# Kernel optimization log

Measured on AMD Instinct MI355X. Metric: run time of the kernel, lower is better.

The kernel has to match this reference:

```python
import jax, jax.numpy as jnp
from jax import lax
import numpy as np

V, Dm, L, B = 32000, 1024, 1024, 4      # vocab, d_model, seq_len, batch
NL, E, H = 2, 8, 1024                    # layers, experts, expert_hidden
DS, DC, EXP = 16, 4, 2                   # d_state, d_conv, expand
DI = EXP * Dm                            # d_inner = 2048
DTR = Dm // 16                           # dt_rank = 64


def setup_inputs() -> dict:
    key = jax.random.key(0)
    ks = iter(jax.random.split(key, 48))
    def n(shape, s=0.02):
        return jax.random.normal(next(ks), shape, jnp.float32) * s
    inp = {
        "tokens": jax.random.randint(next(ks), (B, L), 1, V),
        "emb": jax.random.uniform(next(ks), (V, Dm), jnp.float32, -0.1, 0.1),
        "pos": n((1, L, Dm)),
        # per-layer stacked Mamba params
        "in_w": n((NL, 2 * DI, Dm)),
        "conv_w": n((NL, DI, 1, DC), 0.1),
        "conv_b": jnp.zeros((NL, DI)),
        "xp_w": n((NL, DTR + 2 * DS, DI)),
        "dt_w": n((NL, DI, DTR), 0.1),
        "dt_b": jnp.zeros((NL, DI)),
        "A_log": jnp.log(jnp.tile(jnp.arange(1, DS + 1, dtype=jnp.float32)[None, None, :], (NL, DI, 1))),
        "D_ssm": jnp.ones((NL, DI)),
        "out_w": n((NL, Dm, DI)),
        # layer norms
        "ln1_g": jnp.ones((NL, Dm)), "ln1_b": jnp.zeros((NL, Dm)),
        "ln2_g": jnp.ones((NL, Dm)), "ln2_b": jnp.zeros((NL, Dm)),
        # MoE
        "gate_w": n((NL, E, Dm)), "gate_b": jnp.zeros((NL, E)),
        "e_w1": n((NL, E, H, Dm)), "e_b1": jnp.zeros((NL, E, H)),
        "e_w2": n((NL, E, Dm, H)), "e_b2": jnp.zeros((NL, E, Dm)),
        # head
        "fc1_w": jax.random.uniform(next(ks), (128, Dm), jnp.float32, -0.1, 0.1),
        "fc1_b": jnp.zeros((128,)),
        "fc2_w": jax.random.uniform(next(ks), (2, 128), jnp.float32, -0.1, 0.1),
        "fc2_b": jnp.zeros((2,)),
    }
    return inp


def _ln(x, g, b, eps=1e-5):
    m = x.mean(-1, keepdims=True)
    v = ((x - m) ** 2).mean(-1, keepdims=True)
    return (x - m) * lax.rsqrt(v + eps) * g + b


def _mamba(x, in_w, conv_w, conv_b, xp_w, dt_w, dt_b, A_log, D_ssm, out_w):
    Bb = x.shape[0]
    u, z = jnp.split(x @ in_w.T, 2, axis=-1)  # [B,L,DI] each
    # causal depthwise conv over time
    uc = lax.conv_general_dilated(jnp.swapaxes(u, 1, 2), conv_w, (1,), [(DC - 1, 0)],
                                  feature_group_count=DI,
                                  dimension_numbers=("NCH", "OIH", "NCH")) + conv_b[None, :, None]
    u = jax.nn.silu(jnp.swapaxes(uc, 1, 2))  # [B,L,DI]
    dt, Bm, Cm = jnp.split(u @ xp_w.T, [DTR, DTR + DS], axis=-1)
    dt = jax.nn.softplus(dt @ dt_w.T + dt_b)  # [B,L,DI]
    A = -jnp.exp(A_log)  # [DI,DS]

    def step(h, inp):
        u_t, dt_t, B_t, C_t = inp  # [B,DI],[B,DI],[B,DS],[B,DS]
        h = jnp.exp(dt_t[..., None] * A) * h + (dt_t * u_t)[..., None] * B_t[:, None, :]
        return h, jnp.einsum("bdn,bn->bd", h, C_t)

    h0 = jnp.zeros((Bb, DI, DS), x.dtype)
    xs = tuple(jnp.swapaxes(a, 0, 1) for a in (u, dt, Bm, Cm))
    _, ys = lax.scan(step, h0, xs)
    y = jnp.swapaxes(ys, 0, 1) + u * D_ssm
    return (y * jax.nn.silu(z)) @ out_w.T


def _moe(x, gate_w, gate_b, w1, b1, w2, b2):
    Bb, Ll, Dd = x.shape
    xf = x.reshape(-1, Dd)
    gw = jax.nn.softmax(xf @ gate_w.T + gate_b, axis=-1)  # [N,E]
    top_w = jnp.max(gw, axis=-1)
    top_idx = jnp.argmax(gw, axis=-1)
    out = jnp.zeros_like(xf)
    for e in range(E):  # top-1 routing: only routed tokens keep expert e's output
        ye = jax.nn.relu(xf @ w1[e].T + b1[e]) @ w2[e].T + b2[e]
        out = out + jnp.where((top_idx == e)[:, None], top_w[:, None] * ye, 0.0)
    return out.reshape(Bb, Ll, Dd)


def reference(tokens, emb, pos, in_w, conv_w, conv_b, xp_w, dt_w, dt_b, A_log, D_ssm, out_w,
              ln1_g, ln1_b, ln2_g, ln2_b, gate_w, gate_b, e_w1, e_b1, e_w2, e_b2,
              fc1_w, fc1_b, fc2_w, fc2_b):
    x = emb[tokens] + pos[:, :tokens.shape[1], :]
    for l in range(NL):
        x = x + _ln(_mamba(x, in_w[l], conv_w[l], conv_b[l], xp_w[l], dt_w[l], dt_b[l],
                           A_log[l], D_ssm[l], out_w[l]), ln1_g[l], ln1_b[l])
        x = x + _ln(_moe(x, gate_w[l], gate_b[l], e_w1[l], e_b1[l], e_w2[l], e_b2[l]),
                    ln2_g[l], ln2_b[l])
    mask = (x.sum(-1) != 0)[..., None].astype(x.dtype)
    pooled = (x * mask).sum(1) / jnp.maximum(mask.sum(1), 1.0)
    h = jax.nn.relu(pooled @ fc1_w.T + fc1_b)
    return h @ fc2_w.T + fc2_b
```

## Files before the change

### kernel.cpp

```cpp
#include <hip/hip_runtime.h>
#include <hip/hip_bf16.h>

using bf = __hip_bfloat16;
typedef unsigned short u16;

#define V_   32000
#define DM   1024
#define LQ   1024
#define BB   4
#define NLAY 2
#define NE   8
#define HH   1024
#define DS   16
#define DC   4
#define DI   2048
#define DTR  64
#define NTOK (BB*LQ)

#define NC 8
#define CL (LQ/NC)

typedef __attribute__((ext_vector_type(8))) short s8v;
typedef __attribute__((ext_vector_type(4))) float f4v;

__device__ inline float tofl(float x) { return x; }
__device__ inline float tofl(bf x) { return __bfloat162float(x); }

template<typename T> __device__ inline T fromf(float v);
template<> __device__ inline float fromf<float>(float v) { return v; }
template<> __device__ inline bf fromf<bf>(float v) { return __float2bfloat16(v); }

__device__ inline u16 f2bfu(float x) {
    bf h = __float2bfloat16(x);
    return __builtin_bit_cast(u16, h);
}
__device__ inline float bfu2f(u16 u) {
    bf h = __builtin_bit_cast(bf, u);
    return __bfloat162float(h);
}

__device__ inline f4v mfma16(s8v a, s8v b, f4v c) {
    return __builtin_amdgcn_mfma_f32_16x16x32_bf16(a, b, c, 0, 0, 0);
}

__device__ __forceinline__ void gl2lds16(const u16* g, u16* l) {
    __builtin_amdgcn_global_load_lds(
        (const __attribute__((address_space(1))) unsigned int*)g,
        (__attribute__((address_space(3))) unsigned int*)l, 16, 0, 0);
}

__global__ __launch_bounds__(256) void split2_kernel(
    const float* __restrict__ in, int ldin,
    u16* __restrict__ out, int K)
{
    int id = blockIdx.x * 256 + threadIdx.x;
    int e4 = id * 4;
    int r = e4 / K;
    int k = e4 - r * K;
    float4 v = *(const float4*)(in + (size_t)r * ldin + k);
    int b = k >> 5, j = k & 31;
    ushort4 hi, lo;
    hi.x = f2bfu(v.x); lo.x = f2bfu(v.x - bfu2f(hi.x));
    hi.y = f2bfu(v.y); lo.y = f2bfu(v.y - bfu2f(hi.y));
    hi.z = f2bfu(v.z); lo.z = f2bfu(v.z - bfu2f(hi.z));
    hi.w = f2bfu(v.w); lo.w = f2bfu(v.w - bfu2f(hi.w));
    u16* o = out + (size_t)r * (2 * K) + b * 64 + j;
    *(ushort4*)o = hi;
    *(ushort4*)(o + 32) = lo;
}

__global__ __launch_bounds__(256) void zerof4_kernel(float4* __restrict__ p) {
    p[(size_t)blockIdx.x * 256 + threadIdx.x] = make_float4(0.f, 0.f, 0.f, 0.f);
}

template<typename TC, int TERMS, int BN>
__global__ __launch_bounds__(256, 3) void gemm_s(
    const u16* __restrict__ A, int lda,
    const u16* __restrict__ Bw, int ldb,
    TC* __restrict__ C, int ldc,
    int M, int N, int K32,
    const float* __restrict__ bias, int epi,
    const int* __restrict__ cnt, const int* __restrict__ offs,
    const int* __restrict__ perm, int permmode,
    const float* __restrict__ scale,
    long long strideB_e, long long stride_bias_e,
    int nqz, int atomic_out)
{
    int zb = blockIdx.z;
    int Meff = M, rowoff = 0;
    int q0 = 0, q1 = K32;
    if (cnt) {
        Meff = cnt[zb];
        rowoff = offs[zb];
        Bw += (size_t)zb * strideB_e;
        if (bias) bias += (size_t)zb * stride_bias_e;
    } else if (nqz) {
        q0 = zb * nqz; q1 = q0 + nqz;
    }
    int m0 = blockIdx.y * 128;
    if (m0 >= Meff) return;
    int n0 = blockIdx.x * BN;

    constexpr int MI  = (BN == 128) ? 4 : 2;
    constexpr int NBR = BN / 64;

    __shared__ u16 AsH[128 * 32];
    __shared__ u16 AsL[(TERMS == 3) ? 128 * 32 : 8];
    __shared__ u16 BsH[BN * 32];
    __shared__ u16 BsL[BN * 32];

    int t = threadIdx.x, lane = t & 63, wv = t >> 6;
    int wm = (BN == 128) ? (wv & 1) * 64 : wv * 32;
    int wn = (BN == 128) ? (wv >> 1) * 64 : 0;
    int fr = lane & 15, kq = lane >> 4;
    int chunk = lane & 3;

    int arow[2], brow[2];
#pragma unroll
    for (int r = 0; r < 2; r++) {
        int m = m0 + r * 64 + wv * 16 + (lane >> 2);
        int ar = rowoff + ((m < Meff) ? m : 0);
        arow[r] = (permmode & 1) ? perm[ar] : ar;
    }
#pragma unroll
    for (int r = 0; r < NBR; r++) {
        int n = n0 + r * 64 + wv * 16 + (lane >> 2);
        brow[r] = (n < N) ? n : 0;
    }

    f4v acc[MI][4];
#pragma unroll
    for (int i = 0; i < MI; i++)
#pragma unroll
        for (int j = 0; j < 4; j++) acc[i][j] = 0.f;

    for (int q = q0; q < q1; ++q) {
        size_t acol = (TERMS == 3) ? ((size_t)q * 64 + chunk * 8)
                                   : ((size_t)q * 32 + chunk * 8);
        size_t bcol = (size_t)q * 64 + chunk * 8;
#pragma unroll
        for (int r = 0; r < 2; r++) {
            const u16* ap = A + (size_t)arow[r] * lda + acol;
            gl2lds16(ap, &AsH[(r * 64 + wv * 16) * 32]);
            if constexpr (TERMS == 3)
                gl2lds16(ap + 32, &AsL[(r * 64 + wv * 16) * 32]);
        }
#pragma unroll
        for (int r = 0; r < NBR; r++) {
            const u16* bp = Bw + (size_t)brow[r] * ldb + bcol;
            gl2lds16(bp, &BsH[(r * 64 + wv * 16) * 32]);
            gl2lds16(bp + 32, &BsL[(r * 64 + wv * 16) * 32]);
        }
        __syncthreads();

        s8v ahf[MI], bhf[4], blf[4];
#pragma unroll
        for (int mi = 0; mi < MI; mi++)
            ahf[mi] = *(const s8v*)&AsH[(wm + mi * 16 + fr) * 32 + kq * 8];
#pragma unroll
        for (int ni = 0; ni < 4; ni++)
            bhf[ni] = *(const s8v*)&BsH[(wn + ni * 16 + fr) * 32 + kq * 8];
#pragma unroll
        for (int ni = 0; ni < 4; ni++)
            blf[ni] = *(const s8v*)&BsL[(wn + ni * 16 + fr) * 32 + kq * 8];
#pragma unroll
        for (int mi = 0; mi < MI; mi++)
#pragma unroll
            for (int ni = 0; ni < 4; ni++) {
                acc[mi][ni] = mfma16(ahf[mi], bhf[ni], acc[mi][ni]);
                acc[mi][ni] = mfma16(ahf[mi], blf[ni], acc[mi][ni]);
            }
        if constexpr (TERMS == 3) {
            s8v alf[MI];
#pragma unroll
            for (int mi = 0; mi < MI; mi++)
                alf[mi] = *(const s8v*)&AsL[(wm + mi * 16 + fr) * 32 + kq * 8];
#pragma unroll
            for (int mi = 0; mi < MI; mi++)
#pragma unroll
                for (int ni = 0; ni < 4; ni++)
                    acc[mi][ni] = mfma16(alf[mi], bhf[ni], acc[mi][ni]);
        }
        __syncthreads();
    }

#pragma unroll
    for (int mi = 0; mi < MI; mi++) {
#pragma unroll
        for (int r4 = 0; r4 < 4; r4++) {
            int m = m0 + wm + mi * 16 + kq * 4 + r4;
            if (m >= Meff) continue;
            long long crow;
            float sc = 1.f;
            int ar = rowoff + m;
            if (permmode & 2) { int tok = perm[ar]; crow = tok; sc = scale[tok]; }
            else crow = ar;
#pragma unroll
            for (int ni = 0; ni < 4; ni++) {
                int n = n0 + wn + ni * 16 + fr;
                if (n >= N) continue;
                float v = acc[mi][ni][r4];
                if (bias) v += bias[n];
                if (epi == 1) v = (v > 20.f) ? v : log1pf(__expf(v));
                else if (epi == 2) v = fmaxf(v, 0.f);
                v *= sc;
                long long idx = crow * ldc + n;
                if constexpr (sizeof(TC) == 4) {
                    if (atomic_out) atomicAdd((float*)C + idx, v);
                    else C[idx] = fromf<TC>(v);
                } else {
                    C[idx] = fromf<TC>(v);
                }
            }
        }
    }
}

__global__ __launch_bounds__(256) void embed_kernel(
    const int* __restrict__ tokens, const float* __restrict__ emb,
    const float* __restrict__ pos, float* __restrict__ X)
{
    int id = blockIdx.x * 256 + threadIdx.x;
    int r = id >> 10, d = id & 1023;
    int l = r & (LQ - 1);
    int tok = tokens[r];
    X[id] = emb[(size_t)tok * DM + d] + pos[l * DM + d];
}

__global__ __launch_bounds__(256) void conv_kernel(
    const bf* __restrict__ XZ, const float* __restrict__ cw,
    const float* __restrict__ cb, bf* __restrict__ UC)
{
    int id = blockIdx.x * 256 + threadIdx.x;
    int d = id & (DI - 1);
    int r = id >> 11;
    int l = r & (LQ - 1);
    float acc = cb[d];
#pragma unroll
    for (int j = 0; j < DC; j++) {
        int ll = l - (DC - 1) + j;
        if (ll >= 0)
            acc += tofl(XZ[(size_t)(r - (DC - 1) + j) * (2 * DI) + d]) * cw[d * DC + j];
    }
    float sg = 1.f / (1.f + __expf(-acc));
    UC[id] = __float2bfloat16(acc * sg);
}

template<int PHASE>
__global__ __launch_bounds__(256) void scan_chunk(
    const bf* __restrict__ UC, float* __restrict__ DT,
    const float* __restrict__ W96, const bf* __restrict__ XZ,
    const float* __restrict__ A_log, const float* __restrict__ D_ssm,
    float* __restrict__ Hout, float* __restrict__ Stot,
    const float* __restrict__ Hin)
{
    int d = blockIdx.x * 256 + threadIdx.x;
    int c = blockIdx.y, b = blockIdx.z;
    float A[DS];
#pragma unroll
    for (int n = 0; n < DS; n++) A[n] = -__expf(A_log[d * DS + n]);
    float Dv = D_ssm[d];
    float h[DS];
    size_t hbase = ((size_t)(b * DI + d) * NC + c) * DS;
    if (PHASE == 0) {
#pragma unroll
        for (int n = 0; n < DS; n++) h[n] = 0.f;
    } else {
#pragma unroll
        for (int n = 0; n < DS; n += 4)
            *(float4*)&h[n] = *(const float4*)&Hin[hbase + n];
    }
    float S = 0.f;

    for (int t = 0; t < CL; t++) {
        int r = (b << 10) + c * CL + t;
        float u = tofl(UC[(size_t)r * DI + d]);
        float dt = DT[(size_t)r * DI + d];
        float du = dt * u;
        if (PHASE == 0) S += dt;
        float y = 0.f;
#pragma unroll
        for (int n = 0; n < DS; n++) {
            float Bv = W96[r * 96 + DTR + n];
            h[n] = __expf(dt * A[n]) * h[n] + du * Bv;
            if (PHASE == 1) y += h[n] * W96[r * 96 + DTR + DS + n];
        }
        if (PHASE == 1) {
            float z = tofl(XZ[(size_t)r * (2 * DI) + DI + d]);
            float sil = z / (1.f + __expf(-z));
            DT[(size_t)r * DI + d] = (y + u * Dv) * sil;
        }
    }
    if (PHASE == 0) {
#pragma unroll
        for (int n = 0; n < DS; n += 4)
            *(float4*)&Hout[hbase + n] = *(const float4*)&h[n];
        Stot[(size_t)(b * DI + d) * NC + c] = S;
    }
}

__global__ __launch_bounds__(256) void scan_combine(
    const float* __restrict__ Hout, const float* __restrict__ Stot,
    const float* __restrict__ A_log, float* __restrict__ Hin)
{
    int id = blockIdx.x * 256 + threadIdx.x;
    int n = id & (DS - 1);
    int d = (id >> 4) & (DI - 1);
    int b = id >> 15;
    float A = -__expf(A_log[d * DS + n]);
    float h = 0.f;
    size_t base = (size_t)(b * DI + d) * NC * DS + n;
    size_t sbase = (size_t)(b * DI + d) * NC;
    for (int c = 0; c < NC; c++) {
        Hin[base + (size_t)c * DS] = h;
        h = __expf(A * Stot[sbase + c]) * h + Hout[base + (size_t)c * DS];
    }
}

__global__ __launch_bounds__(256) void ln_residual_kernel(
    float* __restrict__ X, const float* __restrict__ src,
    const float* __restrict__ g, const float* __restrict__ b)
{
    int row = blockIdx.x, tid = threadIdx.x;
    __shared__ float red[256];
    float v[4];
    float s = 0.f;
#pragma unroll
    for (int i = 0; i < 4; i++) { v[i] = src[(size_t)row * DM + tid + 256 * i]; s += v[i]; }
    red[tid] = s; __syncthreads();
    for (int o = 128; o > 0; o >>= 1) { if (tid < o) red[tid] += red[tid + o]; __syncthreads(); }
    float mean = red[0] * (1.f / DM);
    __syncthreads();
    float vs = 0.f;
#pragma unroll
    for (int i = 0; i < 4; i++) { float dd = v[i] - mean; vs += dd * dd; }
    red[tid] = vs; __syncthreads();
    for (int o = 128; o > 0; o >>= 1) { if (tid < o) red[tid] += red[tid + o]; __syncthreads(); }
    float rstd = rsqrtf(red[0] * (1.f / DM) + 1e-5f);
#pragma unroll
    for (int i = 0; i < 4; i++) {
        int c = tid + 256 * i;
        X[(size_t)row * DM + c] += (v[i] - mean) * rstd * g[c] + b[c];
    }
}

__global__ __launch_bounds__(64) void gate_kernel(
    const float* __restrict__ X, const float* __restrict__ gw, const float* __restrict__ gb,
    int* __restrict__ top_idx, float* __restrict__ top_w, int* __restrict__ cnt)
{
    int n = blockIdx.x;
    int lane = threadIdx.x;
    float acc[NE] = {};
    for (int k = lane; k < DM; k += 64) {
        float xv = X[(size_t)n * DM + k];
#pragma unroll
        for (int e = 0; e < NE; e++) acc[e] += xv * gw[e * DM + k];
    }
#pragma unroll
    for (int e = 0; e < NE; e++)
        for (int o = 32; o > 0; o >>= 1) acc[e] += __shfl_down(acc[e], o);
    if (lane == 0) {
        float logits[NE];
        float best = -1e30f; int bi = 0;
#pragma unroll
        for (int e = 0; e < NE; e++) {
            logits[e] = acc[e] + gb[e];
            if (logits[e] > best) { best = logits[e]; bi = e; }
        }
        float s = 0.f;
#pragma unroll
        for (int e = 0; e < NE; e++) s += __expf(logits[e] - best);
        top_idx[n] = bi;
        top_w[n] = 1.f / s;
        atomicAdd(&cnt[bi], 1);
    }
}

__global__ void zero8_kernel(int* p) { if (threadIdx.x < 8) p[threadIdx.x] = 0; }

__global__ void offsets_kernel(const int* __restrict__ cnt, int* __restrict__ offs, int* __restrict__ pos)
{
    if (threadIdx.x == 0) {
        int a = 0;
        for (int e = 0; e < NE; e++) { offs[e] = a; a += cnt[e]; pos[e] = 0; }
        offs[NE] = a;
    }
}

__global__ __launch_bounds__(256) void scatter_kernel(
    const int* __restrict__ top_idx, const int* __restrict__ offs,
    int* __restrict__ pos, int* __restrict__ perm)
{
    int n = blockIdx.x * 256 + threadIdx.x;
    if (n >= NTOK) return;
    int e = top_idx[n];
    int slot = atomicAdd(&pos[e], 1);
    perm[offs[e] + slot] = n;
}

__global__ __launch_bounds__(256) void rowmask_kernel(const float* __restrict__ X, float* __restrict__ maskf)
{
    int row = blockIdx.x, tid = threadIdx.x;
    __shared__ float red[256];
    float s = 0.f;
    for (int i = tid; i < DM; i += 256) s += X[(size_t)row * DM + i];
    red[tid] = s; __syncthreads();
    for (int o = 128; o > 0; o >>= 1) { if (tid < o) red[tid] += red[tid + o]; __syncthreads(); }
    if (tid == 0) maskf[row] = (red[0] != 0.f) ? 1.f : 0.f;
}

__global__ __launch_bounds__(256) void cntb_kernel(const float* __restrict__ maskf, float* __restrict__ cntb)
{
    int b = blockIdx.x, tid = threadIdx.x;
    __shared__ float red[256];
    float s = 0.f;
    for (int i = tid; i < LQ; i += 256) s += maskf[b * LQ + i];
    red[tid] = s; __syncthreads();
    for (int o = 128; o > 0; o >>= 1) { if (tid < o) red[tid] += red[tid + o]; __syncthreads(); }
    if (tid == 0) cntb[b] = red[0];
}

__global__ __launch_bounds__(256) void pooled_kernel(
    const float* __restrict__ X, const float* __restrict__ maskf,
    const float* __restrict__ cntb, float* __restrict__ pooled)
{
    int d = blockIdx.x * 256 + threadIdx.x;
    int b = blockIdx.y;
    float s = 0.f;
    for (int l = 0; l < LQ; l++)
        s += X[(size_t)((b << 10) + l) * DM + d] * maskf[(b << 10) + l];
    pooled[b * DM + d] = s / fmaxf(cntb[b], 1.f);
}

__global__ __launch_bounds__(128) void head_kernel(
    const float* __restrict__ pooled,
    const float* __restrict__ fc1w, const float* __restrict__ fc1b,
    const float* __restrict__ fc2w, const float* __restrict__ fc2b,
    float* __restrict__ out)
{
    int b = blockIdx.x;
    int j = threadIdx.x;
    __shared__ float hbuf[128];
    float acc = fc1b[j];
    for (int k = 0; k < DM; k++) acc += pooled[b * DM + k] * fc1w[j * DM + k];
    hbuf[j] = fmaxf(acc, 0.f);
    __syncthreads();
    if (j < 2) {
        float o = fc2b[j];
        for (int k = 0; k < 128; k++) o += hbuf[k] * fc2w[j * 128 + k];
        out[b * 2 + j] = o;
    }
}

extern "C" void kernel_launch(void* const* d_in, const int* in_sizes, int n_in,
                              void* d_out, int out_size, void* d_ws, size_t ws_size,
                              hipStream_t stream)
{
    const int*   tokens = (const int*)d_in[0];
    const float* emb    = (const float*)d_in[1];
    const float* pos    = (const float*)d_in[2];
    const float* in_w   = (const float*)d_in[3];
    const float* conv_w = (const float*)d_in[4];
    const float* conv_b = (const float*)d_in[5];
    const float* xp_w   = (const float*)d_in[6];
    const float* dt_w   = (const float*)d_in[7];
    const float* dt_b   = (const float*)d_in[8];
    const float* A_log  = (const float*)d_in[9];
    const float* D_ssm  = (const float*)d_in[10];
    const float* out_w  = (const float*)d_in[11];
    const float* ln1_g  = (const float*)d_in[12];
    const float* ln1_b  = (const float*)d_in[13];
    const float* ln2_g  = (const float*)d_in[14];
    const float* ln2_b  = (const float*)d_in[15];
    const float* gate_w = (const float*)d_in[16];
    const float* gate_b = (const float*)d_in[17];
    const float* e_w1   = (const float*)d_in[18];
    const float* e_b1   = (const float*)d_in[19];
    const float* e_w2   = (const float*)d_in[20];
    const float* e_b2   = (const float*)d_in[21];
    const float* fc1_w  = (const float*)d_in[22];
    const float* fc1_b  = (const float*)d_in[23];
    const float* fc2_w  = (const float*)d_in[24];
    const float* fc2_b  = (const float*)d_in[25];
    float* outp = (float*)d_out;

    char* wsb = (char*)d_ws;
    size_t off = 0;
    auto alloc = [&](size_t bytes) { char* p = wsb + off; off += (bytes + 255) & ~(size_t)255; return p; };
    float* X    = (float*)alloc((size_t)NTOK * DM * 4);
    char* xzraw = (char*)alloc((size_t)NTOK * 2 * DI * 2);
    char* ucraw = (char*)alloc((size_t)NTOK * DI * 2);
    float* W96  = (float*)alloc((size_t)NTOK * 96 * 4);
    char* dtraw = (char*)alloc((size_t)NTOK * DI * 4);
    float* Hout = (float*)alloc((size_t)BB * DI * NC * DS * 4);
    float* Hin  = (float*)alloc((size_t)BB * DI * NC * DS * 4);
    float* Stot = (float*)alloc((size_t)BB * DI * NC * 4);
    float* top_w  = (float*)alloc(NTOK * 4);
    float* maskf  = (float*)alloc(NTOK * 4);
    float* pooled = (float*)alloc(BB * DM * 4);
    float* cntb   = (float*)alloc(64);
    int* top_idx  = (int*)alloc(NTOK * 4);
    int* perm     = (int*)alloc(NTOK * 4);
    int* cnt      = (int*)alloc(64);
    int* offs     = (int*)alloc(64);
    int* posc     = (int*)alloc(64);

    bf*    XZ   = (bf*)xzraw;
    bf*    UC   = (bf*)ucraw;
    float* DT   = (float*)dtraw;
    u16*   XS   = (u16*)ucraw;
    u16*   DTS  = (u16*)xzraw;
    float* H1   = (float*)xzraw;
    u16*   H1S  = (u16*)(xzraw + (size_t)NTOK * HH * 4);
    float* MAM1 = (float*)ucraw;
    float* MAM2 = (float*)xzraw;
    u16*   WB   = (u16*)dtraw;
    u16*   WDT  = (u16*)Hin;
    u16*   W96S = (u16*)Hout;

    embed_kernel<<<(NTOK * DM) / 256, 256, 0, stream>>>(tokens, emb, pos, X);

    for (int lay = 0; lay < NLAY; lay++) {
        const float* in_w_l   = in_w   + (size_t)lay * 2 * DI * DM;
        const float* conv_w_l = conv_w + (size_t)lay * DI * DC;
        const float* conv_b_l = conv_b + (size_t)lay * DI;
        const float* xp_w_l   = xp_w   + (size_t)lay * 96 * DI;
        const float* dt_w_l   = dt_w   + (size_t)lay * DI * DTR;
        const float* dt_b_l   = dt_b   + (size_t)lay * DI;
        const float* A_log_l  = A_log  + (size_t)lay * DI * DS;
        const float* D_ssm_l  = D_ssm  + (size_t)lay * DI;
        const float* out_w_l  = out_w  + (size_t)lay * DM * DI;
        const float* gate_w_l = gate_w + (size_t)lay * NE * DM;
        const float* gate_b_l = gate_b + (size_t)lay * NE;
        const float* e_w1_l   = e_w1   + (size_t)lay * NE * HH * DM;
        const float* e_b1_l   = e_b1   + (size_t)lay * NE * HH;
        const float* e_w2_l   = e_w2   + (size_t)lay * NE * DM * HH;
        const float* e_b2_l   = e_b2   + (size_t)lay * NE * DM;

        split2_kernel<<<(NTOK * DM) / 1024, 256, 0, stream>>>(X, DM, XS, DM);
        split2_kernel<<<(2 * DI * DM) / 1024, 256, 0, stream>>>(in_w_l, DM, WB, DM);
        gemm_s<bf, 3, 128><<<dim3(32, 32, 1), 256, 0, stream>>>(
            XS, 2 * DM, WB, 2 * DM, XZ, 2 * DI, NTOK, 2 * DI, DM / 32,
            nullptr, 0, nullptr, nullptr, nullptr, 0, nullptr, 0, 0, 0, 0);

        conv_kernel<<<(NTOK * DI) / 256, 256, 0, stream>>>(XZ, conv_w_l, conv_b_l, UC);

        zerof4_kernel<<<(NTOK * 96) / 1024, 256, 0, stream>>>((float4*)W96);
        split2_kernel<<<(96 * DI) / 1024, 256, 0, stream>>>(xp_w_l, DI, WB, DI);
        gemm_s<float, 2, 128><<<dim3(1, 32, 8), 256, 0, stream>>>(
            (const u16*)UC, DI, WB, 2 * DI, W96, 96, NTOK, 96, DI / 32,
            nullptr, 0, nullptr, nullptr, nullptr, 0, nullptr, 0, 0, (DI / 32) / 8, 1);

        split2_kernel<<<(DI * DTR) / 1024, 256, 0, stream>>>(dt_w_l, DTR, WDT, DTR);
        split2_kernel<<<(NTOK * DTR) / 1024, 256, 0, stream>>>(W96, 96, W96S, DTR);
        gemm_s<float, 3, 128><<<dim3(16, 32, 1), 256, 0, stream>>>(
            W96S, 2 * DTR, WDT, 2 * DTR, DT, DI, NTOK, DI, DTR / 32,
            dt_b_l, 1, nullptr, nullptr, nullptr, 0, nullptr, 0, 0, 0, 0);

        scan_chunk<0><<<dim3(DI / 256, NC, BB), 256, 0, stream>>>(
            UC, DT, W96, XZ, A_log_l, D_ssm_l, Hout, Stot, nullptr);
        scan_combine<<<(BB * DI * DS) / 256, 256, 0, stream>>>(Hout, Stot, A_log_l, Hin);
        scan_chunk<1><<<dim3(DI / 256, NC, BB), 256, 0, stream>>>(
            UC, DT, W96, XZ, A_log_l, D_ssm_l, Hout, Stot, Hin);

        split2_kernel<<<(NTOK * DI) / 1024, 256, 0, stream>>>(DT, DI, DTS, DI);
        split2_kernel<<<(DM * DI) / 1024, 256, 0, stream>>>(out_w_l, DI, WB, DI);
        gemm_s<float, 3, 64><<<dim3(16, 32, 1), 256, 0, stream>>>(
            DTS, 2 * DI, WB, 2 * DI, MAM1, DM, NTOK, DM, DI / 32,
            nullptr, 0, nullptr, nullptr, nullptr, 0, nullptr, 0, 0, 0, 0);

        ln_residual_kernel<<<NTOK, 256, 0, stream>>>(X, MAM1, ln1_g + lay * DM, ln1_b + lay * DM);

        zero8_kernel<<<1, 32, 0, stream>>>(cnt);
        gate_kernel<<<NTOK, 64, 0, stream>>>(X, gate_w_l, gate_b_l, top_idx, top_w, cnt);
        offsets_kernel<<<1, 1, 0, stream>>>(cnt, offs, posc);
        scatter_kernel<<<NTOK / 256, 256, 0, stream>>>(top_idx, offs, posc, perm);

        split2_kernel<<<(NTOK * DM) / 1024, 256, 0, stream>>>(X, DM, XS, DM);
        split2_kernel<<<((size_t)NE * HH * DM) / 1024, 256, 0, stream>>>(e_w1_l, DM, WB, DM);
        gemm_s<float, 3, 64><<<dim3(16, 32, NE), 256, 0, stream>>>(
            XS, 2 * DM, WB, 2 * DM, H1, HH, NTOK, HH, DM / 32,
            e_b1_l, 2, cnt, offs, perm, 1, nullptr,
            (long long)HH * 2 * DM, (long long)HH, 0, 0);

        split2_kernel<<<(NTOK * HH) / 1024, 256, 0, stream>>>(H1, HH, H1S, HH);
        split2_kernel<<<((size_t)NE * DM * HH) / 1024, 256, 0, stream>>>(e_w2_l, HH, WB, HH);
        gemm_s<float, 3, 64><<<dim3(16, 32, NE), 256, 0, stream>>>(
            H1S, 2 * HH, WB, 2 * HH, MAM2, DM, NTOK, DM, HH / 32,
            e_b2_l, 0, cnt, offs, perm, 2, top_w,
            (long long)DM * 2 * HH, (long long)DM, 0, 0);

        ln_residual_kernel<<<NTOK, 256, 0, stream>>>(X, MAM2, ln2_g + lay * DM, ln2_b + lay * DM);
    }

    rowmask_kernel<<<NTOK, 256, 0, stream>>>(X, maskf);
    cntb_kernel<<<BB, 256, 0, stream>>>(maskf, cntb);
    pooled_kernel<<<dim3(DM / 256, BB, 1), 256, 0, stream>>>(X, maskf, cntb, pooled);
    head_kernel<<<BB, 128, 0, stream>>>(pooled, fc1_w, fc1_b, fc2_w, fc2_b, outp);
}
```

Baseline: 1.881 ms.

## Add pipelined in-proj GEMM, fuse bf16 splits into epilogues, widen scan chunks

Adds a 512-thread, 256x128-tile GEMM for the input projection. It uses triple-buffered direct global-to-LDS loads, swizzled LDS reads and raised priority around the MFMA block. The hi/lo bf16 split of the activations moves into the layernorm-residual epilogue and the expert-1 GEMM epilogue, which removes separate split passes and the H1 fp32 buffer. Counter zeroing is folded into layernorm, the scan uses 16 chunks with next-step loads prefetched, and the out-proj and expert GEMMs use BN=128 tiles. The new GEMM drops bounds checks, so it assumes tile-divisible shapes.

```diff
diff --git a/kernel.cpp b/kernel.cpp
--- a/kernel.cpp
+++ b/kernel.cpp
@@ -17,7 +17,7 @@
 #define DTR  64
 #define NTOK (BB*LQ)
 
-#define NC 8
+#define NC 16
 #define CL (LQ/NC)
 
 typedef __attribute__((ext_vector_type(8))) short s8v;
@@ -73,7 +73,98 @@
     p[(size_t)blockIdx.x * 256 + threadIdx.x] = make_float4(0.f, 0.f, 0.f, 0.f);
 }
 
-template<typename TC, int TERMS, int BN>
+__global__ __launch_bounds__(512) void gemm_pipe3(
+    const u16* __restrict__ A, int lda,
+    const u16* __restrict__ Bw, int ldb,
+    bf* __restrict__ C, int ldc,
+    int K32)
+{
+    __shared__ u16 LA[3][256 * 64];
+    __shared__ u16 LB[3][128 * 64];
+
+    int t = threadIdx.x, lane = t & 63, wv = t >> 6;
+    int m0 = blockIdx.y * 256, n0 = blockIdx.x * 128;
+    int wm = (wv >> 1) * 64, wn = (wv & 1) * 64;
+    int fr = lane & 15, kq = lane >> 4;
+
+    int lrow8 = lane >> 3;
+    int lchunk = (lane & 7) ^ lrow8;
+    const u16* Abase = A + (size_t)(m0 + wv * 32 + lrow8) * lda + lchunk * 8;
+    const u16* Bbase = Bw + (size_t)(n0 + wv * 16 + lrow8) * ldb + lchunk * 8;
+
+    f4v acc[4][4];
+#pragma unroll
+    for (int i = 0; i < 4; i++)
+#pragma unroll
+        for (int j = 0; j < 4; j++) acc[i][j] = 0.f;
+
+    auto stage = [&](int q, int s) {
+        const u16* ap = Abase + (size_t)q * 64;
+#pragma unroll
+        for (int j = 0; j < 4; j++)
+            gl2lds16(ap + (size_t)(j * 8) * lda, &LA[s][(wv * 32 + j * 8) * 64]);
+        const u16* bp = Bbase + (size_t)q * 64;
+#pragma unroll
+        for (int j = 0; j < 2; j++)
+            gl2lds16(bp + (size_t)(j * 8) * ldb, &LB[s][(wv * 16 + j * 8) * 64]);
+    };
+
+    stage(0, 0);
+    stage(1, 1);
+
+    for (int q = 0; q < K32; ++q) {
+        int s = q % 3;
+        if (q + 1 < K32) asm volatile("s_waitcnt vmcnt(6)" ::: "memory");
+        else             asm volatile("s_waitcnt vmcnt(0)" ::: "memory");
+        __builtin_amdgcn_sched_barrier(0);
+        __builtin_amdgcn_s_barrier();
+        __builtin_amdgcn_sched_barrier(0);
+
+        if (q + 2 < K32) stage(q + 2, (q + 2) % 3);
+
+        s8v ah[4], al[4], bh[4], bl[4];
+#pragma unroll
+        for (int mi = 0; mi < 4; mi++) {
+            int R = wm + mi * 16 + fr;
+            int c = kq ^ (R & 7);
+            ah[mi] = *(const s8v*)&LA[s][R * 64 + c * 8];
+            al[mi] = *(const s8v*)&LA[s][R * 64 + (c ^ 4) * 8];
+        }
+#pragma unroll
+        for (int ni = 0; ni < 4; ni++) {
+            int R = wn + ni * 16 + fr;
+            int c = kq ^ (R & 7);
+            bh[ni] = *(const s8v*)&LB[s][R * 64 + c * 8];
+            bl[ni] = *(const s8v*)&LB[s][R * 64 + (c ^ 4) * 8];
+        }
+        __builtin_amdgcn_s_setprio(1);
+#pragma unroll
+        for (int mi = 0; mi < 4; mi++)
+#pragma unroll
+            for (int ni = 0; ni < 4; ni++) {
+                acc[mi][ni] = mfma16(ah[mi], bh[ni], acc[mi][ni]);
+                acc[mi][ni] = mfma16(ah[mi], bl[ni], acc[mi][ni]);
+                acc[mi][ni] = mfma16(al[mi], bh[ni], acc[mi][ni]);
+            }
+        __builtin_amdgcn_s_setprio(0);
+        __builtin_amdgcn_sched_barrier(0);
+    }
+
+#pragma unroll
+    for (int mi = 0; mi < 4; mi++) {
+#pragma unroll
+        for (int r4 = 0; r4 < 4; r4++) {
+            int m = m0 + wm + mi * 16 + kq * 4 + r4;
+#pragma unroll
+            for (int ni = 0; ni < 4; ni++) {
+                int n = n0 + wn + ni * 16 + fr;
+                C[(size_t)m * ldc + n] = __float2bfloat16(acc[mi][ni][r4]);
+            }
+        }
+    }
+}
+
+template<typename TC, int TERMS, int BN, int SPLITOUT = 0>
 __global__ __launch_bounds__(256, 3) void gemm_s(
     const u16* __restrict__ A, int lda,
     const u16* __restrict__ Bw, int ldb,
@@ -204,12 +295,20 @@
                 if (epi == 1) v = (v > 20.f) ? v : log1pf(__expf(v));
                 else if (epi == 2) v = fmaxf(v, 0.f);
                 v *= sc;
-                long long idx = crow * ldc + n;
-                if constexpr (sizeof(TC) == 4) {
-                    if (atomic_out) atomicAdd((float*)C + idx, v);
-                    else C[idx] = fromf<TC>(v);
+                if constexpr (SPLITOUT) {
+                    u16 hi = f2bfu(v);
+                    u16 lo = f2bfu(v - bfu2f(hi));
+                    size_t o = (size_t)crow * ldc + ((n >> 5) << 6) + (n & 31);
+                    ((u16*)C)[o] = hi;
+                    ((u16*)C)[o + 32] = lo;
                 } else {
-                    C[idx] = fromf<TC>(v);
+                    long long idx = crow * ldc + n;
+                    if constexpr (sizeof(TC) == 4) {
+                        if (atomic_out) atomicAdd((float*)C + idx, v);
+                        else C[idx] = fromf<TC>(v);
+                    } else {
+                        C[idx] = fromf<TC>(v);
+                    }
                 }
             }
         }
@@ -272,24 +371,32 @@
     }
     float S = 0.f;
 
+    size_t rowb = (size_t)((b << 10) + c * CL);
+    float u_c = tofl(UC[rowb * DI + d]);
+    float dt_c = DT[rowb * DI + d];
+
     for (int t = 0; t < CL; t++) {
-        int r = (b << 10) + c * CL + t;
-        float u = tofl(UC[(size_t)r * DI + d]);
-        float dt = DT[(size_t)r * DI + d];
-        float du = dt * u;
-        if (PHASE == 0) S += dt;
+        size_t r = rowb + t;
+        float u_n = 0.f, dt_n = 0.f;
+        if (t + 1 < CL) {
+            u_n = tofl(UC[(r + 1) * DI + d]);
+            dt_n = DT[(r + 1) * DI + d];
+        }
+        float du = dt_c * u_c;
+        if (PHASE == 0) S += dt_c;
         float y = 0.f;
 #pragma unroll
         for (int n = 0; n < DS; n++) {
             float Bv = W96[r * 96 + DTR + n];
-            h[n] = __expf(dt * A[n]) * h[n] + du * Bv;
+            h[n] = __expf(dt_c * A[n]) * h[n] + du * Bv;
             if (PHASE == 1) y += h[n] * W96[r * 96 + DTR + DS + n];
         }
         if (PHASE == 1) {
-            float z = tofl(XZ[(size_t)r * (2 * DI) + DI + d]);
+            float z = tofl(XZ[r * (2 * DI) + DI + d]);
             float sil = z / (1.f + __expf(-z));
-            DT[(size_t)r * DI + d] = (y + u * Dv) * sil;
-        }
+            DT[r * DI + d] = (y + u_c * Dv) * sil;
+        }
+        u_c = u_n; dt_c = dt_n;
     }
     if (PHASE == 0) {
 #pragma unroll
@@ -319,7 +426,8 @@
 
 __global__ __launch_bounds__(256) void ln_residual_kernel(
     float* __restrict__ X, const float* __restrict__ src,
-    const float* __restrict__ g, const float* __restrict__ b)
+    const float* __restrict__ g, const float* __restrict__ b,
+    u16* __restrict__ xs, int* __restrict__ cntz)
 {
     int row = blockIdx.x, tid = threadIdx.x;
     __shared__ float red[256];
@@ -340,8 +448,17 @@
 #pragma unroll
     for (int i = 0; i < 4; i++) {
         int c = tid + 256 * i;
-        X[(size_t)row * DM + c] += (v[i] - mean) * rstd * g[c] + b[c];
-    }
+        float nx = X[(size_t)row * DM + c] + (v[i] - mean) * rstd * g[c] + b[c];
+        X[(size_t)row * DM + c] = nx;
+        if (xs) {
+            u16 hi = f2bfu(nx);
+            u16 lo = f2bfu(nx - bfu2f(hi));
+            size_t o2 = (size_t)row * (2 * DM) + ((c >> 5) << 6) + (c & 31);
+            xs[o2] = hi;
+            xs[o2 + 32] = lo;
+        }
+    }
+    if (cntz && row == 0 && tid < 8) cntz[tid] = 0;
 }
 
 __global__ __launch_bounds__(64) void gate_kernel(
@@ -375,8 +492,6 @@
         atomicAdd(&cnt[bi], 1);
     }
 }
-
-__global__ void zero8_kernel(int* p) { if (threadIdx.x < 8) p[threadIdx.x] = 0; }
 
 __global__ void offsets_kernel(const int* __restrict__ cnt, int* __restrict__ offs, int* __restrict__ pos)
 {
@@ -510,7 +625,6 @@
     float* DT   = (float*)dtraw;
     u16*   XS   = (u16*)ucraw;
     u16*   DTS  = (u16*)xzraw;
-    float* H1   = (float*)xzraw;
     u16*   H1S  = (u16*)(xzraw + (size_t)NTOK * HH * 4);
     float* MAM1 = (float*)ucraw;
     float* MAM2 = (float*)xzraw;
@@ -537,11 +651,11 @@
         const float* e_w2_l   = e_w2   + (size_t)lay * NE * DM * HH;
         const float* e_b2_l   = e_b2   + (size_t)lay * NE * DM;
 
-        split2_kernel<<<(NTOK * DM) / 1024, 256, 0, stream>>>(X, DM, XS, DM);
+        if (lay == 0)
+            split2_kernel<<<(NTOK * DM) / 1024, 256, 0, stream>>>(X, DM, XS, DM);
         split2_kernel<<<(2 * DI * DM) / 1024, 256, 0, stream>>>(in_w_l, DM, WB, DM);
-        gemm_s<bf, 3, 128><<<dim3(32, 32, 1), 256, 0, stream>>>(
-            XS, 2 * DM, WB, 2 * DM, XZ, 2 * DI, NTOK, 2 * DI, DM / 32,
-            nullptr, 0, nullptr, nullptr, nullptr, 0, nullptr, 0, 0, 0, 0);
+        gemm_pipe3<<<dim3(2 * DI / 128, NTOK / 256, 1), 512, 0, stream>>>(
+            XS, 2 * DM, WB, 2 * DM, XZ, 2 * DI, DM / 32);
 
         conv_kernel<<<(NTOK * DI) / 256, 256, 0, stream>>>(XZ, conv_w_l, conv_b_l, UC);
 
@@ -565,32 +679,31 @@
 
         split2_kernel<<<(NTOK * DI) / 1024, 256, 0, stream>>>(DT, DI, DTS, DI);
         split2_kernel<<<(DM * DI) / 1024, 256, 0, stream>>>(out_w_l, DI, WB, DI);
-        gemm_s<float, 3, 64><<<dim3(16, 32, 1), 256, 0, stream>>>(
+        gemm_s<float, 3, 128><<<dim3(8, 32, 1), 256, 0, stream>>>(
             DTS, 2 * DI, WB, 2 * DI, MAM1, DM, NTOK, DM, DI / 32,
             nullptr, 0, nullptr, nullptr, nullptr, 0, nullptr, 0, 0, 0, 0);
 
-        ln_residual_kernel<<<NTOK, 256, 0, stream>>>(X, MAM1, ln1_g + lay * DM, ln1_b + lay * DM);
-
-        zero8_kernel<<<1, 32, 0, stream>>>(cnt);
+        ln_residual_kernel<<<NTOK, 256, 0, stream>>>(
+            X, MAM1, ln1_g + lay * DM, ln1_b + lay * DM, XS, cnt);
+
         gate_kernel<<<NTOK, 64, 0, stream>>>(X, gate_w_l, gate_b_l, top_idx, top_w, cnt);
         offsets_kernel<<<1, 1, 0, stream>>>(cnt, offs, posc);
         scatter_kernel<<<NTOK / 256, 256, 0, stream>>>(top_idx, offs, posc, perm);
 
-        split2_kernel<<<(NTOK * DM) / 1024, 256, 0, stream>>>(X, DM, XS, DM);
         split2_kernel<<<((size_t)NE * HH * DM) / 1024, 256, 0, stream>>>(e_w1_l, DM, WB, DM);
-        gemm_s<float, 3, 64><<<dim3(16, 32, NE), 256, 0, stream>>>(
-            XS, 2 * DM, WB, 2 * DM, H1, HH, NTOK, HH, DM / 32,
+        gemm_s<u16, 3, 128, 1><<<dim3(8, 32, NE), 256, 0, stream>>>(
+            XS, 2 * DM, WB, 2 * DM, H1S, 2 * HH, NTOK, HH, DM / 32,
             e_b1_l, 2, cnt, offs, perm, 1, nullptr,
             (long long)HH * 2 * DM, (long long)HH, 0, 0);
 
-        split2_kernel<<<(NTOK * HH) / 1024, 256, 0, stream>>>(H1, HH, H1S, HH);
         split2_kernel<<<((size_t)NE * DM * HH) / 1024, 256, 0, stream>>>(e_w2_l, HH, WB, HH);
-        gemm_s<float, 3, 64><<<dim3(16, 32, NE), 256, 0, stream>>>(
+        gemm_s<float, 3, 128><<<dim3(8, 32, NE), 256, 0, stream>>>(
             H1S, 2 * HH, WB, 2 * HH, MAM2, DM, NTOK, DM, HH / 32,
             e_b2_l, 0, cnt, offs, perm, 2, top_w,
             (long long)DM * 2 * HH, (long long)DM, 0, 0);
 
-        ln_residual_kernel<<<NTOK, 256, 0, stream>>>(X, MAM2, ln2_g + lay * DM, ln2_b + lay * DM);
+        ln_residual_kernel<<<NTOK, 256, 0, stream>>>(
+            X, MAM2, ln2_g + lay * DM, ln2_b + lay * DM, XS, nullptr);
     }
 
     rowmask_kernel<<<NTOK, 256, 0, stream>>>(X, maskf);
```

After: 1.803 ms. 1.04x faster.
